# Performance work log

Measured on AMD Instinct MI355X. Metric: run time of the kernel, lower is better.

Reference implementation:

```python
import jax, jax.numpy as jnp
import numpy as np

N_NODES = 100000
N_EDGES = 1600000
IN_DIM = 128
OUT_DIM = 128


def setup_inputs() -> dict:
    key = jax.random.key(0)
    k_x, k_r, k_c, k_v, k_w, k_b = jax.random.split(key, 6)
    x = jax.random.normal(k_x, (N_NODES, IN_DIM), dtype=jnp.float32)
    rows = jax.random.randint(k_r, (N_EDGES,), 0, N_NODES, dtype=jnp.int32)
    cols = jax.random.randint(k_c, (N_EDGES,), 0, N_NODES, dtype=jnp.int32)
    vals = jax.random.uniform(k_v, (N_EDGES,), dtype=jnp.float32)
    # nn.Linear(in_dim, out_dim): kaiming-uniform-ish init, exact values irrelevant
    bound = 1.0 / np.sqrt(IN_DIM)
    W = jax.random.uniform(k_w, (IN_DIM, OUT_DIM), dtype=jnp.float32, minval=-bound, maxval=bound)
    b = jax.random.uniform(k_b, (OUT_DIM,), dtype=jnp.float32, minval=-bound, maxval=bound)
    return {"x": x, "W": W, "b": b, "vals": vals, "rows": rows, "cols": cols}


def reference(x, W, b, vals, rows, cols):
    # x = self.linear(x)
    h = x @ W + b  # [N, out_dim]
    # x = torch.sparse.mm(adj, x): out[r] += vals[e] * h[cols[e]] for each edge e with rows[e]==r
    msgs = vals[:, None] * h[cols]  # [E, out_dim]
    out = jax.ops.segment_sum(msgs, rows, num_segments=N_NODES)  # [N, out_dim]
    return out
```

## Files before the change

### kernel.cpp

```cpp
#include <hip/hip_runtime.h>

#define N_NODES 100000
#define N_EDGES 1600000
#define DIM 128
#define NBKT 782
#define B1   256
#define EPB  6250
#define CAP  2560
#define GEMM_NB 1563

typedef __attribute__((ext_vector_type(8))) short bf16x8;
typedef __attribute__((ext_vector_type(4))) float f32x4;

__device__ __forceinline__ unsigned short f2bf(float f) {
    unsigned u = __float_as_uint(f);
    u += 0x7FFF + ((u >> 16) & 1);
    return (unsigned short)(u >> 16);
}
__device__ __forceinline__ float bflo(unsigned u) { return __uint_as_float(u << 16); }
__device__ __forceinline__ float bfhi(unsigned u) { return __uint_as_float(u & 0xFFFF0000u); }

__global__ __launch_bounds__(256) void wt_pack(const float* __restrict__ W,
                                               uint4* __restrict__ wtf) {
    const int t = blockIdx.x * 256 + threadIdx.x;
    const int f = t >> 6;
    const int l = t & 63;
    const int kc = f >> 3, nt = f & 7;
    const int quad = l >> 4, n = l & 15;
    unsigned o[4];
    #pragma unroll
    for (int jj = 0; jj < 4; ++jj) {
        const int k0 = kc * 32 + quad * 8 + jj * 2;
        const unsigned short lo = f2bf(W[(k0 + 0) * DIM + nt * 16 + n]);
        const unsigned short hi = f2bf(W[(k0 + 1) * DIM + nt * 16 + n]);
        o[jj] = (unsigned)lo | ((unsigned)hi << 16);
    }
    wtf[t] = make_uint4(o[0], o[1], o[2], o[3]);
}

#define ROWSTRIDE 136
__global__ __launch_bounds__(256) void gemm_count(const float* __restrict__ x,
                                                  const uint4* __restrict__ wtf,
                                                  const float* __restrict__ b,
                                                  unsigned short* __restrict__ h,
                                                  const int* __restrict__ rows,
                                                  int* __restrict__ cnt) {
    __shared__ uint4 smem4[4 * 16 * ROWSTRIDE / 8];
    if (blockIdx.x >= GEMM_NB) {
        int* c = (int*)smem4;
        const int k = blockIdx.x - GEMM_NB, t = threadIdx.x;
        for (int bb = t; bb < NBKT; bb += 256) c[bb] = 0;
        __syncthreads();
        const int e0 = k * EPB;
        #pragma unroll
        for (int i = 0; i < 6; ++i) {
            const int4 r4 = *(const int4*)&rows[e0 + (t + i * 256) * 4];
            atomicAdd(&c[r4.x >> 7], 1);
            atomicAdd(&c[r4.y >> 7], 1);
            atomicAdd(&c[r4.z >> 7], 1);
            atomicAdd(&c[r4.w >> 7], 1);
        }
        if (t < EPB - 6144) atomicAdd(&c[rows[e0 + 6144 + t] >> 7], 1);
        __syncthreads();
        for (int bb = t; bb < NBKT; bb += 256) cnt[bb * B1 + k] = c[bb];
        return;
    }

    const int wave = threadIdx.x >> 6;
    const int lane = threadIdx.x & 63;
    const int quad = lane >> 4;
    const int m = lane & 15;
    const int row_base = blockIdx.x * 64 + wave * 16;
    const int row = row_base + m;
    const bool rok = (row < N_NODES);

    uint4 bf[32];
    #pragma unroll
    for (int f = 0; f < 32; ++f) bf[f] = wtf[f * 64 + lane];

    bf16x8 af[4];
    #pragma unroll
    for (int kc = 0; kc < 4; ++kc) {
        float4 v0, v1;
        if (rok) {
            v0 = *(const float4*)&x[(size_t)row * DIM + kc * 32 + quad * 8];
            v1 = *(const float4*)&x[(size_t)row * DIM + kc * 32 + quad * 8 + 4];
        } else {
            v0 = make_float4(0.f, 0.f, 0.f, 0.f);
            v1 = make_float4(0.f, 0.f, 0.f, 0.f);
        }
        union { bf16x8 v; unsigned u[4]; } a;
        a.u[0] = (unsigned)f2bf(v0.x) | ((unsigned)f2bf(v0.y) << 16);
        a.u[1] = (unsigned)f2bf(v0.z) | ((unsigned)f2bf(v0.w) << 16);
        a.u[2] = (unsigned)f2bf(v1.x) | ((unsigned)f2bf(v1.y) << 16);
        a.u[3] = (unsigned)f2bf(v1.z) | ((unsigned)f2bf(v1.w) << 16);
        af[kc] = a.v;
    }

    f32x4 acc[8];
    #pragma unroll
    for (int nt = 0; nt < 8; ++nt) {
        const float bv = b[nt * 16 + m];
        acc[nt] = (f32x4){bv, bv, bv, bv};
    }

    #pragma unroll
    for (int kc = 0; kc < 4; ++kc) {
        #pragma unroll
        for (int nt = 0; nt < 8; ++nt) {
            union { uint4 u; bf16x8 v; } bb; bb.u = bf[kc * 8 + nt];
            acc[nt] = __builtin_amdgcn_mfma_f32_16x16x32_bf16(af[kc], bb.v, acc[nt], 0, 0, 0);
        }
    }

    unsigned short* sh = (unsigned short*)smem4 + wave * 16 * ROWSTRIDE;
    #pragma unroll
    for (int nt = 0; nt < 8; ++nt) {
        #pragma unroll
        for (int i = 0; i < 4; ++i)
            sh[(quad * 4 + i) * ROWSTRIDE + nt * 16 + m] = f2bf(acc[nt][i]);
    }
    __syncthreads();
    uint4* hv4 = (uint4*)h;
    const int seg = lane & 15;
    #pragma unroll
    for (int c = 0; c < 4; ++c) {
        const int rl = (lane >> 4) + c * 4;
        const int r = row_base + rl;
        const uint4 v = *(const uint4*)&sh[rl * ROWSTRIDE + seg * 8];
        if (r < N_NODES) hv4[(size_t)r * 16 + seg] = v;
    }
}

__global__ __launch_bounds__(256) void p1_totals(const int* __restrict__ cnt,
                                                 int* __restrict__ tot) {
    __shared__ int s[256];
    const int t = threadIdx.x, bb = blockIdx.x;
    s[t] = cnt[bb * B1 + t];
    __syncthreads();
    for (int o = 128; o > 0; o >>= 1) {
        if (t < o) s[t] += s[t + o];
        __syncthreads();
    }
    if (t == 0) tot[bb] = s[0];
}

__global__ __launch_bounds__(1024) void p1_scan_tot(const int* __restrict__ tot,
                                                    int* __restrict__ bktbase) {
    __shared__ int s[1024];
    const int t = threadIdx.x;
    const int v = (t < NBKT) ? tot[t] : 0;
    s[t] = v;
    __syncthreads();
    for (int o = 1; o < 1024; o <<= 1) {
        const int add = (t >= o) ? s[t - o] : 0;
        __syncthreads();
        s[t] += add;
        __syncthreads();
    }
    if (t < NBKT) bktbase[t] = s[t] - v;
    if (t == NBKT - 1) bktbase[NBKT] = s[t];
}

__global__ __launch_bounds__(256) void p1_scan_blocks(const int* __restrict__ cnt,
                                                      const int* __restrict__ bktbase,
                                                      int* __restrict__ offs) {
    __shared__ int s[256];
    const int bb = blockIdx.x, t = threadIdx.x;
    const int v = cnt[bb * B1 + t];
    s[t] = v;
    __syncthreads();
    for (int o = 1; o < 256; o <<= 1) {
        const int add = (t >= o) ? s[t - o] : 0;
        __syncthreads();
        s[t] += add;
        __syncthreads();
    }
    offs[bb * B1 + t] = bktbase[bb] + s[t] - v;
}

__global__ __launch_bounds__(256) void p1_scatter(const int* __restrict__ rows,
                                                  const int* __restrict__ cols,
                                                  const float* __restrict__ vals,
                                                  const int* __restrict__ offs,
                                                  int2* __restrict__ binned) {
    __shared__ int cur[NBKT];
    const int k = blockIdx.x, t = threadIdx.x;
    for (int bb = t; bb < NBKT; bb += 256) cur[bb] = offs[bb * B1 + k];
    __syncthreads();
    const int e0 = k * EPB;
    #pragma unroll
    for (int i = 0; i < 6; ++i) {
        const int g = (t + i * 256) * 4;
        const int4   r4 = *(const int4*)&rows[e0 + g];
        const int4   c4 = *(const int4*)&cols[e0 + g];
        const float4 v4 = *(const float4*)&vals[e0 + g];
        int p;
        p = atomicAdd(&cur[r4.x >> 7], 1);
        binned[p] = make_int2(((r4.x & 127) << 24) | c4.x, __float_as_int(v4.x));
        p = atomicAdd(&cur[r4.y >> 7], 1);
        binned[p] = make_int2(((r4.y & 127) << 24) | c4.y, __float_as_int(v4.y));
        p = atomicAdd(&cur[r4.z >> 7], 1);
        binned[p] = make_int2(((r4.z & 127) << 24) | c4.z, __float_as_int(v4.z));
        p = atomicAdd(&cur[r4.w >> 7], 1);
        binned[p] = make_int2(((r4.w & 127) << 24) | c4.w, __float_as_int(v4.w));
    }
    if (t < EPB - 6144) {
        const int e = e0 + 6144 + t;
        const int r = rows[e];
        const int p = atomicAdd(&cur[r >> 7], 1);
        binned[p] = make_int2(((r & 127) << 24) | cols[e], __float_as_int(vals[e]));
    }
}

__global__ __launch_bounds__(512) void p2_gather(const unsigned* __restrict__ h32,
                                                 const int2* __restrict__ binned,
                                                 const int* __restrict__ bktbase,
                                                 float* __restrict__ out) {
    __shared__ int2 ebuf[CAP];
    __shared__ int rcount[128], rstart[128], rcur[128], sscan[128];
    const int b = blockIdx.x, t = threadIdx.x;
    const int s0 = bktbase[b];
    const int n = bktbase[b + 1] - s0;

    int2 ereg[5];
    int nm = 0;
    #pragma unroll
    for (int jj = 0; jj < 5; ++jj) {
        const int j = t + jj * 512;
        if (j < n) { ereg[jj] = binned[s0 + j]; nm = jj + 1; }
    }

    if (t < 128) rcount[t] = 0;
    __syncthreads();
    #pragma unroll
    for (int jj = 0; jj < 5; ++jj)
        if (jj < nm) atomicAdd(&rcount[((unsigned)ereg[jj].x) >> 24], 1);
    __syncthreads();

    if (t < 128) sscan[t] = rcount[t];
    __syncthreads();
    for (int o = 1; o < 128; o <<= 1) {
        const int add = (t < 128 && t >= o) ? sscan[t - o] : 0;
        __syncthreads();
        if (t < 128) sscan[t] += add;
        __syncthreads();
    }
    if (t < 128) { rstart[t] = sscan[t] - rcount[t]; rcur[t] = sscan[t] - rcount[t]; }
    __syncthreads();

    #pragma unroll
    for (int jj = 0; jj < 5; ++jj)
        if (jj < nm) {
            const int lr = ((unsigned)ereg[jj].x) >> 24;
            const int pos = atomicAdd(&rcur[lr], 1);
            ebuf[pos] = make_int2(ereg[jj].x & 0x00FFFFFF, ereg[jj].y);
        }
    __syncthreads();

    const int wave = t >> 6, lane = t & 63;
    const char* hbase = (const char*)h32;
    const unsigned lane4 = (unsigned)lane * 4u;

    for (int i = 0; i < 8; ++i) {
        const int lr0 = wave * 16 + i;
        const int lr1 = lr0 + 8;
        const int r0 = b * 128 + lr0;
        const int r1 = b * 128 + lr1;
        const int st0 = rstart[lr0], cn0 = rcount[lr0];
        const int st1 = rstart[lr1], cn1 = rcount[lr1];

        float a0x = 0.f, a0y = 0.f, c0x = 0.f, c0y = 0.f;
        float a1x = 0.f, a1y = 0.f, c1x = 0.f, c1y = 0.f;
        int j0 = 0, j1 = 0;

        while (j0 + 2 <= cn0 && j1 + 2 <= cn1) {
            const int2 e0 = ebuf[st0 + j0], e1 = ebuf[st0 + j0 + 1];
            const int2 f0 = ebuf[st1 + j1], f1 = ebuf[st1 + j1 + 1];
            const unsigned u0 = *(const unsigned*)(hbase + ((((unsigned)e0.x) << 8) | lane4));
            const unsigned u1 = *(const unsigned*)(hbase + ((((unsigned)e1.x) << 8) | lane4));
            const unsigned w0 = *(const unsigned*)(hbase + ((((unsigned)f0.x) << 8) | lane4));
            const unsigned w1 = *(const unsigned*)(hbase + ((((unsigned)f1.x) << 8) | lane4));
            const float v0 = __int_as_float(e0.y), v1 = __int_as_float(e1.y);
            const float s0v = __int_as_float(f0.y), s1v = __int_as_float(f1.y);
            a0x = fmaf(v0, bflo(u0), a0x);  a0y = fmaf(v0, bfhi(u0), a0y);
            c0x = fmaf(v1, bflo(u1), c0x);  c0y = fmaf(v1, bfhi(u1), c0y);
            a1x = fmaf(s0v, bflo(w0), a1x); a1y = fmaf(s0v, bfhi(w0), a1y);
            c1x = fmaf(s1v, bflo(w1), c1x); c1y = fmaf(s1v, bfhi(w1), c1y);
            j0 += 2; j1 += 2;
        }
        for (; j0 + 2 <= cn0; j0 += 2) {
            const int2 e0 = ebuf[st0 + j0], e1 = ebuf[st0 + j0 + 1];
            const unsigned u0 = *(const unsigned*)(hbase + ((((unsigned)e0.x) << 8) | lane4));
            const unsigned u1 = *(const unsigned*)(hbase + ((((unsigned)e1.x) << 8) | lane4));
            const float v0 = __int_as_float(e0.y), v1 = __int_as_float(e1.y);
            a0x = fmaf(v0, bflo(u0), a0x); a0y = fmaf(v0, bfhi(u0), a0y);
            c0x = fmaf(v1, bflo(u1), c0x); c0y = fmaf(v1, bfhi(u1), c0y);
        }
        if (j0 < cn0) {
            const int2 e0 = ebuf[st0 + j0];
            const unsigned u0 = *(const unsigned*)(hbase + ((((unsigned)e0.x) << 8) | lane4));
            const float v0 = __int_as_float(e0.y);
            a0x = fmaf(v0, bflo(u0), a0x); a0y = fmaf(v0, bfhi(u0), a0y);
        }
        for (; j1 + 2 <= cn1; j1 += 2) {
            const int2 f0 = ebuf[st1 + j1], f1 = ebuf[st1 + j1 + 1];
            const unsigned w0 = *(const unsigned*)(hbase + ((((unsigned)f0.x) << 8) | lane4));
            const unsigned w1 = *(const unsigned*)(hbase + ((((unsigned)f1.x) << 8) | lane4));
            const float s0v = __int_as_float(f0.y), s1v = __int_as_float(f1.y);
            a1x = fmaf(s0v, bflo(w0), a1x); a1y = fmaf(s0v, bfhi(w0), a1y);
            c1x = fmaf(s1v, bflo(w1), c1x); c1y = fmaf(s1v, bfhi(w1), c1y);
        }
        if (j1 < cn1) {
            const int2 f0 = ebuf[st1 + j1];
            const unsigned w0 = *(const unsigned*)(hbase + ((((unsigned)f0.x) << 8) | lane4));
            const float s0v = __int_as_float(f0.y);
            a1x = fmaf(s0v, bflo(w0), a1x); a1y = fmaf(s0v, bfhi(w0), a1y);
        }

        if (r0 < N_NODES) {
            float2 o; o.x = a0x + c0x; o.y = a0y + c0y;
            *(float2*)&out[(size_t)r0 * DIM + lane * 2] = o;
        }
        if (r1 < N_NODES) {
            float2 o; o.x = a1x + c1x; o.y = a1y + c1y;
            *(float2*)&out[(size_t)r1 * DIM + lane * 2] = o;
        }
    }
}

extern "C" void kernel_launch(void* const* d_in, const int* in_sizes, int n_in,
                              void* d_out, int out_size, void* d_ws, size_t ws_size,
                              hipStream_t stream) {
    const float* x    = (const float*)d_in[0];
    const float* W    = (const float*)d_in[1];
    const float* b    = (const float*)d_in[2];
    const float* vals = (const float*)d_in[3];
    const int*   rows = (const int*)d_in[4];
    const int*   cols = (const int*)d_in[5];
    float* out = (float*)d_out;

    char* ws = (char*)d_ws;
    unsigned short* h = (unsigned short*)(ws + 0);
    uint4* wtf    = (uint4*)(ws + 25600000);
    int*   cnt    = (int*)  (ws + 25632768);
    int*   offs   = (int*)  (ws + 26433536);
    int*   tot    = (int*)  (ws + 27234304);
    int*   bktbase= (int*)  (ws + 27237440);
    int2*  binned = (int2*) (ws + 27240576);

    wt_pack<<<8, 256, 0, stream>>>(W, wtf);

    gemm_count<<<GEMM_NB + B1, 256, 0, stream>>>(x, wtf, b, h, rows, cnt);

    p1_totals<<<NBKT, 256, 0, stream>>>(cnt, tot);
    p1_scan_tot<<<1, 1024, 0, stream>>>(tot, bktbase);
    p1_scan_blocks<<<NBKT, 256, 0, stream>>>(cnt, bktbase, offs);

    p1_scatter<<<B1, 256, 0, stream>>>(rows, cols, vals, offs, binned);

    p2_gather<<<NBKT, 512, 0, stream>>>((const unsigned*)h, binned, bktbase, out);
}
```

Measured before the change: 225.7 us.

## Halve bucket size and replace per-block offset scans with global atomic cursors

Row buckets shrink from 128 to 64 rows, doubling the number of gather blocks, and the gather block drops to 256 threads with a smaller shared edge buffer. The two-level count/scan (per-block counts, totals, block scans) becomes one set of global atomic counters, a single scan kernel, and atomic reservation of bucket ranges inside the scatter kernel, which recounts its edges locally. This removes two kernel launches and the large count/offset arrays, in exchange for global atomics, a redundant local histogram pass in scatter, and bucket order inside each bin that is no longer deterministic.

```diff
diff --git a/kernel.cpp b/kernel.cpp
--- a/kernel.cpp
+++ b/kernel.cpp
@@ -3,10 +3,10 @@
 #define N_NODES 100000
 #define N_EDGES 1600000
 #define DIM 128
-#define NBKT 782
+#define NBKT 1563
 #define B1   256
 #define EPB  6250
-#define CAP  2560
+#define CAP2 1408
 #define GEMM_NB 1563
 
 typedef __attribute__((ext_vector_type(8))) short bf16x8;
@@ -21,8 +21,10 @@
 __device__ __forceinline__ float bfhi(unsigned u) { return __uint_as_float(u & 0xFFFF0000u); }
 
 __global__ __launch_bounds__(256) void wt_pack(const float* __restrict__ W,
-                                               uint4* __restrict__ wtf) {
+                                               uint4* __restrict__ wtf,
+                                               int* __restrict__ gcnt) {
     const int t = blockIdx.x * 256 + threadIdx.x;
+    if (t < NBKT) gcnt[t] = 0;
     const int f = t >> 6;
     const int l = t & 63;
     const int kc = f >> 3, nt = f & 7;
@@ -44,7 +46,7 @@
                                                   const float* __restrict__ b,
                                                   unsigned short* __restrict__ h,
                                                   const int* __restrict__ rows,
-                                                  int* __restrict__ cnt) {
+                                                  int* __restrict__ gcnt) {
     __shared__ uint4 smem4[4 * 16 * ROWSTRIDE / 8];
     if (blockIdx.x >= GEMM_NB) {
         int* c = (int*)smem4;
@@ -55,14 +57,17 @@
         #pragma unroll
         for (int i = 0; i < 6; ++i) {
             const int4 r4 = *(const int4*)&rows[e0 + (t + i * 256) * 4];
-            atomicAdd(&c[r4.x >> 7], 1);
-            atomicAdd(&c[r4.y >> 7], 1);
-            atomicAdd(&c[r4.z >> 7], 1);
-            atomicAdd(&c[r4.w >> 7], 1);
-        }
-        if (t < EPB - 6144) atomicAdd(&c[rows[e0 + 6144 + t] >> 7], 1);
-        __syncthreads();
-        for (int bb = t; bb < NBKT; bb += 256) cnt[bb * B1 + k] = c[bb];
+            atomicAdd(&c[r4.x >> 6], 1);
+            atomicAdd(&c[r4.y >> 6], 1);
+            atomicAdd(&c[r4.z >> 6], 1);
+            atomicAdd(&c[r4.w >> 6], 1);
+        }
+        if (t < EPB - 6144) atomicAdd(&c[rows[e0 + 6144 + t] >> 6], 1);
+        __syncthreads();
+        for (int bb = t; bb < NBKT; bb += 256) {
+            const int v = c[bb];
+            if (v) atomicAdd(&gcnt[bb], v);
+        }
         return;
     }
 
@@ -132,25 +137,15 @@
     }
 }
 
-__global__ __launch_bounds__(256) void p1_totals(const int* __restrict__ cnt,
-                                                 int* __restrict__ tot) {
-    __shared__ int s[256];
-    const int t = threadIdx.x, bb = blockIdx.x;
-    s[t] = cnt[bb * B1 + t];
-    __syncthreads();
-    for (int o = 128; o > 0; o >>= 1) {
-        if (t < o) s[t] += s[t + o];
-        __syncthreads();
-    }
-    if (t == 0) tot[bb] = s[0];
-}
-
-__global__ __launch_bounds__(1024) void p1_scan_tot(const int* __restrict__ tot,
-                                                    int* __restrict__ bktbase) {
+__global__ __launch_bounds__(1024) void p1_scan(const int* __restrict__ gcnt,
+                                                int* __restrict__ bktbase,
+                                                int* __restrict__ gcur) {
     __shared__ int s[1024];
     const int t = threadIdx.x;
-    const int v = (t < NBKT) ? tot[t] : 0;
-    s[t] = v;
+    const int i0 = 2 * t, i1 = 2 * t + 1;
+    const int x0 = (i0 < NBKT) ? gcnt[i0] : 0;
+    const int x1 = (i1 < NBKT) ? gcnt[i1] : 0;
+    s[t] = x0 + x1;
     __syncthreads();
     for (int o = 1; o < 1024; o <<= 1) {
         const int add = (t >= o) ? s[t - o] : 0;
@@ -158,37 +153,40 @@
         s[t] += add;
         __syncthreads();
     }
-    if (t < NBKT) bktbase[t] = s[t] - v;
-    if (t == NBKT - 1) bktbase[NBKT] = s[t];
-}
-
-__global__ __launch_bounds__(256) void p1_scan_blocks(const int* __restrict__ cnt,
-                                                      const int* __restrict__ bktbase,
-                                                      int* __restrict__ offs) {
-    __shared__ int s[256];
-    const int bb = blockIdx.x, t = threadIdx.x;
-    const int v = cnt[bb * B1 + t];
-    s[t] = v;
-    __syncthreads();
-    for (int o = 1; o < 256; o <<= 1) {
-        const int add = (t >= o) ? s[t - o] : 0;
-        __syncthreads();
-        s[t] += add;
-        __syncthreads();
-    }
-    offs[bb * B1 + t] = bktbase[bb] + s[t] - v;
+    const int excl = s[t] - x0 - x1;
+    if (i0 < NBKT) { bktbase[i0] = excl; gcur[i0] = excl; }
+    if (i1 <= NBKT) {
+        bktbase[i1] = excl + x0;
+        if (i1 < NBKT) gcur[i1] = excl + x0;
+    }
 }
 
 __global__ __launch_bounds__(256) void p1_scatter(const int* __restrict__ rows,
                                                   const int* __restrict__ cols,
                                                   const float* __restrict__ vals,
-                                                  const int* __restrict__ offs,
+                                                  int* __restrict__ gcur,
                                                   int2* __restrict__ binned) {
+    __shared__ int c[NBKT];
     __shared__ int cur[NBKT];
     const int k = blockIdx.x, t = threadIdx.x;
-    for (int bb = t; bb < NBKT; bb += 256) cur[bb] = offs[bb * B1 + k];
+    for (int bb = t; bb < NBKT; bb += 256) c[bb] = 0;
     __syncthreads();
     const int e0 = k * EPB;
+    #pragma unroll
+    for (int i = 0; i < 6; ++i) {
+        const int4 r4 = *(const int4*)&rows[e0 + (t + i * 256) * 4];
+        atomicAdd(&c[r4.x >> 6], 1);
+        atomicAdd(&c[r4.y >> 6], 1);
+        atomicAdd(&c[r4.z >> 6], 1);
+        atomicAdd(&c[r4.w >> 6], 1);
+    }
+    if (t < EPB - 6144) atomicAdd(&c[rows[e0 + 6144 + t] >> 6], 1);
+    __syncthreads();
+    for (int bb = t; bb < NBKT; bb += 256) {
+        const int cc = c[bb];
+        if (cc) cur[bb] = atomicAdd(&gcur[bb], cc);
+    }
+    __syncthreads();
     #pragma unroll
     for (int i = 0; i < 6; ++i) {
         const int g = (t + i * 256) * 4;
@@ -196,61 +194,61 @@
         const int4   c4 = *(const int4*)&cols[e0 + g];
         const float4 v4 = *(const float4*)&vals[e0 + g];
         int p;
-        p = atomicAdd(&cur[r4.x >> 7], 1);
-        binned[p] = make_int2(((r4.x & 127) << 24) | c4.x, __float_as_int(v4.x));
-        p = atomicAdd(&cur[r4.y >> 7], 1);
-        binned[p] = make_int2(((r4.y & 127) << 24) | c4.y, __float_as_int(v4.y));
-        p = atomicAdd(&cur[r4.z >> 7], 1);
-        binned[p] = make_int2(((r4.z & 127) << 24) | c4.z, __float_as_int(v4.z));
-        p = atomicAdd(&cur[r4.w >> 7], 1);
-        binned[p] = make_int2(((r4.w & 127) << 24) | c4.w, __float_as_int(v4.w));
+        p = atomicAdd(&cur[r4.x >> 6], 1);
+        binned[p] = make_int2(((r4.x & 63) << 24) | c4.x, __float_as_int(v4.x));
+        p = atomicAdd(&cur[r4.y >> 6], 1);
+        binned[p] = make_int2(((r4.y & 63) << 24) | c4.y, __float_as_int(v4.y));
+        p = atomicAdd(&cur[r4.z >> 6], 1);
+        binned[p] = make_int2(((r4.z & 63) << 24) | c4.z, __float_as_int(v4.z));
+        p = atomicAdd(&cur[r4.w >> 6], 1);
+        binned[p] = make_int2(((r4.w & 63) << 24) | c4.w, __float_as_int(v4.w));
     }
     if (t < EPB - 6144) {
         const int e = e0 + 6144 + t;
         const int r = rows[e];
-        const int p = atomicAdd(&cur[r >> 7], 1);
-        binned[p] = make_int2(((r & 127) << 24) | cols[e], __float_as_int(vals[e]));
-    }
-}
-
-__global__ __launch_bounds__(512) void p2_gather(const unsigned* __restrict__ h32,
+        const int p = atomicAdd(&cur[r >> 6], 1);
+        binned[p] = make_int2(((r & 63) << 24) | cols[e], __float_as_int(vals[e]));
+    }
+}
+
+__global__ __launch_bounds__(256) void p2_gather(const unsigned* __restrict__ h32,
                                                  const int2* __restrict__ binned,
                                                  const int* __restrict__ bktbase,
                                                  float* __restrict__ out) {
-    __shared__ int2 ebuf[CAP];
-    __shared__ int rcount[128], rstart[128], rcur[128], sscan[128];
+    __shared__ int2 ebuf[CAP2];
+    __shared__ int rcount[64], rstart[64], rcur[64], sscan[64];
     const int b = blockIdx.x, t = threadIdx.x;
     const int s0 = bktbase[b];
     const int n = bktbase[b + 1] - s0;
 
-    int2 ereg[5];
+    int2 ereg[6];
     int nm = 0;
     #pragma unroll
-    for (int jj = 0; jj < 5; ++jj) {
-        const int j = t + jj * 512;
+    for (int jj = 0; jj < 6; ++jj) {
+        const int j = t + jj * 256;
         if (j < n) { ereg[jj] = binned[s0 + j]; nm = jj + 1; }
     }
 
-    if (t < 128) rcount[t] = 0;
-    __syncthreads();
-    #pragma unroll
-    for (int jj = 0; jj < 5; ++jj)
+    if (t < 64) rcount[t] = 0;
+    __syncthreads();
+    #pragma unroll
+    for (int jj = 0; jj < 6; ++jj)
         if (jj < nm) atomicAdd(&rcount[((unsigned)ereg[jj].x) >> 24], 1);
     __syncthreads();
 
-    if (t < 128) sscan[t] = rcount[t];
-    __syncthreads();
-    for (int o = 1; o < 128; o <<= 1) {
-        const int add = (t < 128 && t >= o) ? sscan[t - o] : 0;
-        __syncthreads();
-        if (t < 128) sscan[t] += add;
-        __syncthreads();
-    }
-    if (t < 128) { rstart[t] = sscan[t] - rcount[t]; rcur[t] = sscan[t] - rcount[t]; }
-    __syncthreads();
-
-    #pragma unroll
-    for (int jj = 0; jj < 5; ++jj)
+    if (t < 64) sscan[t] = rcount[t];
+    __syncthreads();
+    for (int o = 1; o < 64; o <<= 1) {
+        const int add = (t < 64 && t >= o) ? sscan[t - o] : 0;
+        __syncthreads();
+        if (t < 64) sscan[t] += add;
+        __syncthreads();
+    }
+    if (t < 64) { rstart[t] = sscan[t] - rcount[t]; rcur[t] = sscan[t] - rcount[t]; }
+    __syncthreads();
+
+    #pragma unroll
+    for (int jj = 0; jj < 6; ++jj)
         if (jj < nm) {
             const int lr = ((unsigned)ereg[jj].x) >> 24;
             const int pos = atomicAdd(&rcur[lr], 1);
@@ -265,8 +263,8 @@
     for (int i = 0; i < 8; ++i) {
         const int lr0 = wave * 16 + i;
         const int lr1 = lr0 + 8;
-        const int r0 = b * 128 + lr0;
-        const int r1 = b * 128 + lr1;
+        const int r0 = b * 64 + lr0;
+        const int r1 = b * 64 + lr1;
         const int st0 = rstart[lr0], cn0 = rcount[lr0];
         const int st1 = rstart[lr1], cn1 = rcount[lr1];
 
@@ -343,21 +341,18 @@
     char* ws = (char*)d_ws;
     unsigned short* h = (unsigned short*)(ws + 0);
     uint4* wtf    = (uint4*)(ws + 25600000);
-    int*   cnt    = (int*)  (ws + 25632768);
-    int*   offs   = (int*)  (ws + 26433536);
-    int*   tot    = (int*)  (ws + 27234304);
-    int*   bktbase= (int*)  (ws + 27237440);
-    int2*  binned = (int2*) (ws + 27240576);
-
-    wt_pack<<<8, 256, 0, stream>>>(W, wtf);
-
-    gemm_count<<<GEMM_NB + B1, 256, 0, stream>>>(x, wtf, b, h, rows, cnt);
-
-    p1_totals<<<NBKT, 256, 0, stream>>>(cnt, tot);
-    p1_scan_tot<<<1, 1024, 0, stream>>>(tot, bktbase);
-    p1_scan_blocks<<<NBKT, 256, 0, stream>>>(cnt, bktbase, offs);
-
-    p1_scatter<<<B1, 256, 0, stream>>>(rows, cols, vals, offs, binned);
-
-    p2_gather<<<NBKT, 512, 0, stream>>>((const unsigned*)h, binned, bktbase, out);
-}
+    int*   gcnt   = (int*)  (ws + 25632768);
+    int*   bktbase= (int*)  (ws + 25639024);
+    int*   gcur   = (int*)  (ws + 25645280);
+    int2*  binned = (int2*) (ws + 25651536);
+
+    wt_pack<<<8, 256, 0, stream>>>(W, wtf, gcnt);
+
+    gemm_count<<<GEMM_NB + B1, 256, 0, stream>>>(x, wtf, b, h, rows, gcnt);
+
+    p1_scan<<<1, 1024, 0, stream>>>(gcnt, bktbase, gcur);
+
+    p1_scatter<<<B1, 256, 0, stream>>>(rows, cols, vals, gcur, binned);
+
+    p2_gather<<<NBKT, 256, 0, stream>>>((const unsigned*)h, binned, bktbase, out);
+}
```

Measured after the change: 229.9 us. About the same (+1.8%).
